# Optimization experiments

Hardware: AMD Instinct MI355X
Metric: run time of the kernel (lower is better)

## Reference

```python
import jax, jax.numpy as jnp
import numpy as np

B, L, D_IN, H, N2, NL, D_OUT = 32, 4096, 16, 128, 32, 4, 8


def setup_inputs() -> dict:
    key = jax.random.key(0)
    ks = jax.random.split(key, 12)
    x = jax.random.normal(ks[0], (B, L, D_IN), jnp.float32)
    times = jax.random.uniform(ks[1], (B, L), jnp.float32)
    enc_w = jax.random.normal(ks[2], (H, D_IN), jnp.float32) / np.sqrt(D_IN)
    enc_b = jnp.zeros((H,), jnp.float32)
    # S4D kernel params per layer (stacked along NL)
    log_dt = jax.random.uniform(ks[3], (NL, H), jnp.float32) * (np.log(0.1) - np.log(0.001)) + np.log(0.001)
    log_A_real = jnp.full((NL, H, N2), np.log(0.5), jnp.float32)
    A_imag = jnp.broadcast_to(np.pi * jnp.arange(N2, dtype=jnp.float32), (NL, H, N2)).astype(jnp.float32)
    C_re = jax.random.normal(ks[4], (NL, H, N2), jnp.float32) * (0.5 ** 0.5)
    C_im = jax.random.normal(ks[5], (NL, H, N2), jnp.float32) * (0.5 ** 0.5)
    D = jax.random.normal(ks[6], (NL, H), jnp.float32)
    conv_w = jax.random.normal(ks[7], (NL, 2 * H, H), jnp.float32) / np.sqrt(H)  # 1x1 conv
    conv_b = jnp.zeros((NL, 2 * H), jnp.float32)
    ln_w = jnp.ones((NL, H), jnp.float32)
    ln_b = jnp.zeros((NL, H), jnp.float32)
    dec_w = jax.random.normal(ks[8], (D_OUT, H), jnp.float32) / np.sqrt(H)
    dec_b = jnp.zeros((D_OUT,), jnp.float32)
    return dict(x=x, times=times, enc_w=enc_w, enc_b=enc_b, log_dt=log_dt,
                log_A_real=log_A_real, A_imag=A_imag, C_re=C_re, C_im=C_im, D=D,
                conv_w=conv_w, conv_b=conv_b, ln_w=ln_w, ln_b=ln_b, dec_w=dec_w, dec_b=dec_b)


def _s4d_kernel(log_dt, log_A_real, A_imag, C_re, C_im, L_):
    # Vandermonde construction of the S4D convolution kernel, shape (H, L)
    dt = jnp.exp(log_dt)[:, None]                      # (H, 1)
    A = -jnp.exp(log_A_real) + 1j * A_imag             # (H, N2)
    dtA = A * dt                                       # (H, N2)
    C = (C_re + 1j * C_im) * (jnp.exp(dtA) - 1.0) / A  # (H, N2)
    K = jnp.exp(dtA[:, :, None] * jnp.arange(L_))      # (H, N2, L)
    return 2.0 * jnp.einsum('hn,hnl->hl', C, K).real


def _layernorm(x, w, b, eps=1e-5):
    mu = x.mean(-1, keepdims=True)
    var = ((x - mu) ** 2).mean(-1, keepdims=True)
    return (x - mu) * jax.lax.rsqrt(var + eps) * w + b


def _forward(x, enc_w, enc_b, log_dt, log_A_real, A_imag, C_re, C_im, D,
             conv_w, conv_b, ln_w, ln_b, dec_w, dec_b):
    L_ = x.shape[1]
    u = jnp.transpose(x @ enc_w.T + enc_b, (0, 2, 1))  # (B, H, L)
    for l in range(NL):
        z = u
        k = _s4d_kernel(log_dt[l], log_A_real[l], A_imag[l], C_re[l], C_im[l], L_)  # (H, L)
        # FFT-based causal convolution with zero padding to 2L
        k_f = jnp.fft.rfft(k, n=2 * L_)                # (H, L+1)
        u_f = jnp.fft.rfft(z, n=2 * L_)                # (B, H, L+1)
        y = jnp.fft.irfft(u_f * k_f, n=2 * L_)[..., :L_]
        y = y + z * D[l][:, None]                      # skip term
        y = jax.nn.gelu(y, approximate=False)          # torch nn.GELU = exact erf
        # 1x1 conv to 2H channels then GLU over channel dim
        v = jnp.einsum('oh,bhl->bol', conv_w[l], y) + conv_b[l][:, None]
        a, g = jnp.split(v, 2, axis=1)
        y = a * jax.nn.sigmoid(g)
        u = y + u                                      # residual
        u = jnp.transpose(_layernorm(jnp.transpose(u, (0, 2, 1)), ln_w[l], ln_b[l]), (0, 2, 1))  # postnorm
    emb = jnp.transpose(u, (0, 2, 1))                  # (B, L, H)
    pooled = emb.mean(axis=1)                          # (B, H)
    pred = jax.nn.sigmoid(pooled @ dec_w.T + dec_b)    # (B, D_OUT)
    return pred, emb


def reference(x, times, enc_w, enc_b, log_dt, log_A_real, A_imag, C_re, C_im, D,
              conv_w, conv_b, ln_w, ln_b, dec_w, dec_b):
    # times is accepted but unused, matching the original forward signature
    return _forward(x, enc_w, enc_b, log_dt, log_A_real, A_imag, C_re, C_im, D,
                    conv_w, conv_b, ln_w, ln_b, dec_w, dec_b)
```

## Files before the change

kernel.cpp:

```cpp
#include <hip/hip_runtime.h>
#include <hip/hip_bf16.h>

#define B_ 32
#define L_ 4096
#define DIN 16
#define H_ 128
#define N2_ 32
#define NL_ 4
#define CL 64
#define NC 64

#define OFF_U   ((size_t)0)
#define SZ_U    ((size_t)B_*H_*L_/2)
#define OFF_Y   (OFF_U + SZ_U)
#define SZ_Y    ((size_t)B_*H_*L_/2)
#define OFF_T1  (OFF_Y + SZ_Y)
#define SZ_T1   ((size_t)NL_*H_*64*64)
#define OFF_K   (OFF_T1 + SZ_T1)
#define SZ_K    ((size_t)NL_*H_*64)
#define OFF_CP  (OFF_K + SZ_K)
#define SZ_CP   ((size_t)NL_*H_*64)
#define OFF_W64 (OFF_CP + SZ_CP)
#define SZ_W64  ((size_t)NL_*H_*64)
#define OFF_W5  (OFF_W64 + SZ_W64)
#define SZ_W5   ((size_t)NL_*H_*64)
#define OFF_DTA (OFF_W5 + SZ_W5)
#define SZ_DTA  ((size_t)NL_*H_*N2_*4)
#define OFF_PL  (OFF_DTA + SZ_DTA)
#define SZ_PL   ((size_t)B_*H_)
#define OFF_WB  (OFF_PL + SZ_PL)
#define SZ_WB   ((size_t)NL_*256*128/2)
#define OFF_T1F (OFF_WB + SZ_WB)
#define SZ_TF   ((size_t)NL_*H_*4096)
#define OFF_TKF (OFF_T1F + SZ_TF)
#define OFF_T2F (OFF_TKF + SZ_TF)

#define ZP 72
#define EP 68

typedef __bf16 bf16_t;
typedef bf16_t bf16x8 __attribute__((ext_vector_type(8)));
typedef float f32x4 __attribute__((ext_vector_type(4)));
typedef unsigned short u16x8 __attribute__((ext_vector_type(8)));

#define MFMA(a, b, c) __builtin_amdgcn_mfma_f32_16x16x32_bf16(a, b, c, 0, 0, 0)
#define BCB(v) __builtin_bit_cast(bf16x8, v)

__device__ __forceinline__ unsigned short f2bf(float f) {
    return __builtin_bit_cast(unsigned short, (__bf16)f);
}
__device__ __forceinline__ float bf2f(unsigned short u) {
    return __builtin_bit_cast(float, (unsigned int)u << 16);
}
__device__ __forceinline__ void store_hl(unsigned short* p, int idx, float v) {
    unsigned short hi = f2bf(v);
    p[idx]     = hi;
    p[idx + 8] = f2bf(v - bf2f(hi));
}
__device__ __forceinline__ float gelu_f(float a) {
    float uu = a * fmaf(0.0356774081f, a * a, 0.7978845608f);
    float e  = __expf(2.0f * uu);
    float th = 1.0f - 2.0f / (e + 1.0f);
    return 0.5f * a * (1.0f + th);
}
__device__ __forceinline__ int yswz(int l, int h) {
    return (l * 128 + h) ^ ((l & 7) << 3);
}

__global__ __launch_bounds__(256) void prep_params(const float* log_dt, const float* log_A_real,
                                                   const float* A_imag, const float* C_re,
                                                   const float* C_im, float* ws) {
    int idx = blockIdx.x * 256 + threadIdx.x;
    if (idx >= NL_ * H_ * N2_) return;
    int n  = idx & 31;
    int lh = idx >> 5;

    float dt  = expf(log_dt[lh]);
    float Are = -expf(log_A_real[idx]);
    float Aim = A_imag[idx];
    float dre = Are * dt, dim = Aim * dt;
    float er  = expf(dre);
    float sw, cw; sincosf(dim, &sw, &cw);
    float wre = er * cw, wim = er * sw;
    float nre = wre - 1.0f, nim = wim;
    float den = Are * Are + Aim * Aim;
    float qre = (nre * Are + nim * Aim) / den;
    float qim = (nim * Are - nre * Aim) / den;
    float cre = C_re[idx], cim = C_im[idx];

    float* cp  = ws + OFF_CP  + (size_t)lh * 64;
    float* w64 = ws + OFF_W64 + (size_t)lh * 64;
    float* w5  = ws + OFF_W5  + (size_t)lh * 64;
    cp[2 * n]     = cre * qre - cim * qim;
    cp[2 * n + 1] = cre * qim + cim * qre;
    *((float4*)(ws + OFF_DTA) + (size_t)lh * 32 + n) = make_float4(dre, dim, wre, wim);

    float e64 = expf(64.0f * dre);
    float s64, c64; sincosf(64.0f * dim, &s64, &c64);
    float ar = e64 * c64, ai = e64 * s64;
    w64[2 * n] = ar; w64[2 * n + 1] = ai;
    #pragma unroll
    for (int q = 0; q < 3; ++q) {
        float nr = ar * ar - ai * ai;
        float ni = 2.0f * ar * ai;
        ar = nr; ai = ni;
    }
    w5[2 * n] = ar; w5[2 * n + 1] = ai;
}

__global__ __launch_bounds__(256) void prep_pow(float* ws) {
    int idx = blockIdx.x * 256 + threadIdx.x;
    int n  = idx & 31;
    int e  = (idx >> 5) & 63;
    int lh = idx >> 11;
    float4 dw = *((const float4*)(ws + OFF_DTA) + (size_t)lh * 32 + n);
    float ew = expf((float)e * dw.x);
    float sn, cs; sincosf((float)e * dw.y, &sn, &cs);
    float pr = ew * cs, pi = ew * sn;

    float* t1 = ws + OFF_T1 + (size_t)lh * 4096;
    *(float2*)&t1[e * 64 + 2 * n] = make_float2(pr, pi);

    unsigned short* t1f = (unsigned short*)(ws + OFF_T1F) + (size_t)lh * 8192;
    unsigned short* t2f = (unsigned short*)(ws + OFF_T2F) + (size_t)lh * 8192;
    int k1 = 63 - e;
    store_hl(t1f, (k1 >> 3) * 1024 + (2 * n) * 16 + (k1 & 7), pr);
    store_hl(t1f, (k1 >> 3) * 1024 + (2 * n + 1) * 16 + (k1 & 7), pi);
    float qr = pr * dw.z - pi * dw.w;
    float qi = pr * dw.w + pi * dw.z;
    store_hl(t2f, ((2 * n) >> 3) * 1024 + e * 16 + ((2 * n) & 7), qr);
    store_hl(t2f, ((2 * n + 1) >> 3) * 1024 + e * 16 + ((2 * n + 1) & 7), qi);
}

__global__ __launch_bounds__(256) void compute_k(float* ws) {
    int idx = blockIdx.x * 256 + threadIdx.x;
    if (idx >= NL_ * H_ * 64) return;
    int s  = idx & 63;
    int lh = idx >> 6;
    const float* t1 = ws + OFF_T1 + (size_t)lh * 4096 + (size_t)s * 64;
    const float* cp = ws + OFF_CP + (size_t)lh * 64;
    float acc = 0.0f;
    #pragma unroll
    for (int n = 0; n < 32; ++n)
        acc += cp[2 * n] * t1[2 * n] - cp[2 * n + 1] * t1[2 * n + 1];
    ws[OFF_K + (size_t)lh * 64 + s] = 2.0f * acc;
}

__global__ __launch_bounds__(256) void prep_tkf(float* ws) {
    int idx = blockIdx.x * 256 + threadIdx.x;
    int tau = idx & 63;
    int s   = (idx >> 6) & 63;
    int lh  = idx >> 12;
    float v = (tau >= s) ? ws[OFF_K + (size_t)lh * 64 + (tau - s)] : 0.0f;
    unsigned short* dst = (unsigned short*)(ws + OFF_TKF) + (size_t)lh * 8192;
    store_hl(dst, (s >> 3) * 1024 + (s & 7) + tau * 16, v);
}

__global__ __launch_bounds__(256) void prep_wbf(const float* conv_w, float* ws) {
    int i = blockIdx.x * 256 + threadIdx.x;
    ((unsigned short*)(ws + OFF_WB))[i] = f2bf(conv_w[i]);
}

__global__ __launch_bounds__(256) void encoder_kernel(const float* x, const float* enc_w,
                                                      const float* enc_b, float* ws) {
    __shared__ float wlds[H_ * DIN];
    __shared__ float blds[H_];
    int t  = threadIdx.x;
    int b  = blockIdx.x >> 4;
    int l0 = (blockIdx.x & 15) * 256;
    for (int i = t; i < H_ * DIN; i += 256) wlds[i] = enc_w[i];
    if (t < H_) blds[t] = enc_b[t];
    float xr[16];
    const float* xp = x + ((size_t)b * L_ + l0 + t) * DIN;
    #pragma unroll
    for (int d = 0; d < 16; ++d) xr[d] = xp[d];
    __syncthreads();
    unsigned short* u = (unsigned short*)(ws + OFF_U) + (size_t)b * H_ * L_ + l0 + t;
    for (int h = 0; h < H_; ++h) {
        float acc = blds[h];
        #pragma unroll
        for (int d = 0; d < 16; ++d) acc += xr[d] * wlds[h * 16 + d];
        u[(size_t)h * L_] = f2bf(acc);
    }
}

__global__ __launch_bounds__(256) void s4d_mfma(const float* Dp, float* ws, int layer) {
    __shared__ unsigned short zsh[64 * ZP];
    __shared__ float eg[64 * EP];
    __shared__ float tex[8][64];
    __shared__ float bex[8][64];

    int t  = threadIdx.x;
    int b  = blockIdx.x >> 7;
    int h  = blockIdx.x & 127;
    int lh = layer * H_ + h;
    int w  = t >> 6;
    int l  = t & 63;
    int lr = l & 15;
    int lg = l >> 4;

    const unsigned short* ug = (const unsigned short*)(ws + OFF_U) + ((size_t)b * H_ + h) * L_;

    {
        int base = t * 16;
        int c = base >> 6, s0 = base & 63;
        *(u16x8*)&zsh[c * ZP + s0]     = *(const u16x8*)&ug[base];
        *(u16x8*)&zsh[c * ZP + s0 + 8] = *(const u16x8*)&ug[base + 8];
    }

    const unsigned short* t1f = (const unsigned short*)(ws + OFF_T1F) + (size_t)lh * 8192;
    const unsigned short* tkf = (const unsigned short*)(ws + OFF_TKF) + (size_t)lh * 8192;
    const unsigned short* t2f = (const unsigned short*)(ws + OFF_T2F) + (size_t)lh * 8192;
    int bo = lg * 1024 + (w * 16 + lr) * 16;
    bf16x8 T1h0 = BCB(*(const u16x8*)&t1f[bo]);
    bf16x8 T1l0 = BCB(*(const u16x8*)&t1f[bo + 8]);
    bf16x8 T1h1 = BCB(*(const u16x8*)&t1f[bo + 4096]);
    bf16x8 T1l1 = BCB(*(const u16x8*)&t1f[bo + 4096 + 8]);
    bf16x8 TKh0 = BCB(*(const u16x8*)&tkf[bo]);
    bf16x8 TKl0 = BCB(*(const u16x8*)&tkf[bo + 8]);
    bf16x8 TKh1 = BCB(*(const u16x8*)&tkf[bo + 4096]);
    bf16x8 TKl1 = BCB(*(const u16x8*)&tkf[bo + 4096 + 8]);

    f32x4 accE[4], accC[4];
    #pragma unroll
    for (int ct = 0; ct < 4; ++ct) { accE[ct] = (f32x4)0.0f; accC[ct] = (f32x4)0.0f; }

    __syncthreads();

    #pragma unroll
    for (int ct = 0; ct < 4; ++ct) {
        int ar = (ct * 16 + lr) * ZP;
        bf16x8 ah0 = BCB(*(const u16x8*)&zsh[ar + lg * 8]);
        bf16x8 ah1 = BCB(*(const u16x8*)&zsh[ar + 32 + lg * 8]);
        accE[ct] = MFMA(ah0, T1h0, accE[ct]);
        accE[ct] = MFMA(ah0, T1l0, accE[ct]);
        accE[ct] = MFMA(ah1, T1h1, accE[ct]);
        accE[ct] = MFMA(ah1, T1l1, accE[ct]);
        accC[ct] = MFMA(ah0, TKh0, accC[ct]);
        accC[ct] = MFMA(ah0, TKl0, accC[ct]);
        accC[ct] = MFMA(ah1, TKh1, accC[ct]);
        accC[ct] = MFMA(ah1, TKl1, accC[ct]);
    }
    #pragma unroll
    for (int ct = 0; ct < 4; ++ct)
        #pragma unroll
        for (int r = 0; r < 4; ++r)
            eg[(ct * 16 + lg * 4 + r) * EP + w * 16 + lr] = accE[ct][r];

    bf16x8 T2h0 = BCB(*(const u16x8*)&t2f[bo]);
    bf16x8 T2l0 = BCB(*(const u16x8*)&t2f[bo + 8]);
    bf16x8 T2h1 = BCB(*(const u16x8*)&t2f[bo + 4096]);
    bf16x8 T2l1 = BCB(*(const u16x8*)&t2f[bo + 4096 + 8]);
    float zep[16];
    #pragma unroll
    for (int ct = 0; ct < 4; ++ct)
        #pragma unroll
        for (int r = 0; r < 4; ++r) {
            int c = ct * 16 + lg * 4 + r, tau = w * 16 + lr;
            zep[ct * 4 + r] = bf2f(zsh[c * ZP + tau]);
        }
    __syncthreads();

    {
        int n   = t & 31;
        int oct = t >> 5;
        const float* cp   = ws + OFF_CP  + (size_t)lh * 64;
        const float* w64p = ws + OFF_W64 + (size_t)lh * 64;
        const float* w5p  = ws + OFF_W5  + (size_t)lh * 64;
        float cre = cp[2 * n], cim = cp[2 * n + 1];
        float wr  = w64p[2 * n], wi = w64p[2 * n + 1];
        float2 e[8];
        float sre = 0.f, sim = 0.f;
        #pragma unroll
        for (int j = 0; j < 8; ++j) {
            e[j] = *(const float2*)&eg[(8 * oct + j) * EP + 2 * n];
            float nr = fmaf(wr, sre, fmaf(-wi, sim, e[j].x));
            float ni = fmaf(wr, sim, fmaf(wi, sre, e[j].y));
            sre = nr; sim = ni;
        }
        *(float2*)&tex[oct][2 * n] = make_float2(sre, sim);
        __syncthreads();
        if (t < 32) {
            float Wr = w5p[2 * n], Wi = w5p[2 * n + 1];
            float br = 0.f, bi = 0.f;
            #pragma unroll
            for (int o = 0; o < 8; ++o) {
                *(float2*)&bex[o][2 * n] = make_float2(br, bi);
                float2 T = *(const float2*)&tex[o][2 * n];
                float nr = fmaf(Wr, br, fmaf(-Wi, bi, T.x));
                float ni = fmaf(Wr, bi, fmaf(Wi, br, T.y));
                br = nr; bi = ni;
            }
        }
        __syncthreads();
        float2 Sb = *(const float2*)&bex[oct][2 * n];
        sre = Sb.x; sim = Sb.y;
        #pragma unroll
        for (int j = 0; j < 8; ++j) {
            int c = 8 * oct + j;
            float gre = 2.0f * (cre * sre - cim * sim);
            float gim = -2.0f * (cre * sim + cim * sre);
            unsigned int pk = (unsigned int)f2bf(gre) | ((unsigned int)f2bf(gim) << 16);
            *(unsigned int*)&zsh[c * ZP + 2 * n] = pk;
            float nr = fmaf(wr, sre, fmaf(-wi, sim, e[j].x));
            float ni = fmaf(wr, sim, fmaf(wi, sre, e[j].y));
            sre = nr; sim = ni;
        }
    }
    float Dh = Dp[lh];
    __syncthreads();

    #pragma unroll
    for (int ct = 0; ct < 4; ++ct) {
        int ar = (ct * 16 + lr) * ZP;
        bf16x8 gh0 = BCB(*(const u16x8*)&zsh[ar + lg * 8]);
        bf16x8 gh1 = BCB(*(const u16x8*)&zsh[ar + 32 + lg * 8]);
        accC[ct] = MFMA(gh0, T2h0, accC[ct]);
        accC[ct] = MFMA(gh0, T2l0, accC[ct]);
        accC[ct] = MFMA(gh1, T2h1, accC[ct]);
        accC[ct] = MFMA(gh1, T2l1, accC[ct]);
    }

    unsigned short* yb = (unsigned short*)(ws + OFF_Y) + ((size_t)b * H_ + h) * L_;
    #pragma unroll
    for (int ct = 0; ct < 4; ++ct)
        #pragma unroll
        for (int r = 0; r < 4; ++r) {
            float acc = fmaf(Dh, zep[ct * 4 + r], accC[ct][r]);
            yb[(ct * 16 + lg * 4 + r) * 64 + w * 16 + lr] = f2bf(gelu_f(acc));
        }
}

__global__ __launch_bounds__(256) void conv_glu_ln_mfma(const float* conv_b, const float* ln_w,
                                                        const float* ln_b, float* ws, int layer) {
    __shared__ unsigned short yt[64 * 128];
    __shared__ float wsum[4][64];
    __shared__ float wsq[4][64];

    int t    = threadIdx.x;
    int b    = blockIdx.x >> 6;
    int l0   = (blockIdx.x & 63) * 64;
    int w    = t >> 6;
    int lam  = t & 63;
    int g4   = lam >> 4;
    int ncol = lam & 15;

    const unsigned short* yg = (const unsigned short*)(ws + OFF_Y) + (size_t)b * H_ * L_;
    const unsigned short* wb = (const unsigned short*)(ws + OFF_WB) + (size_t)layer * 256 * 128;

    {
        int ll = t & 63;
        int hb = (t >> 6) * 32;
        const unsigned short* ycol = yg + l0 + ll;
        #pragma unroll
        for (int g = 0; g < 4; ++g) {
            u16x8 tmp;
            #pragma unroll
            for (int i = 0; i < 8; ++i)
                tmp[i] = ycol[(size_t)(hb + g * 8 + i) * L_];
            *(u16x8*)&yt[yswz(ll, hb + g * 8)] = tmp;
        }
    }

    const float* cb = conv_b + layer * 256;
    f32x4 dA[2][4], dG[2][4];
    #pragma unroll
    for (int oa = 0; oa < 2; ++oa) {
        int ba = w * 32 + oa * 16 + g4 * 4;
        f32x4 bA, bG;
        #pragma unroll
        for (int r = 0; r < 4; ++r) { bA[r] = cb[ba + r]; bG[r] = cb[128 + ba + r]; }
        #pragma unroll
        for (int nt = 0; nt < 4; ++nt) { dA[oa][nt] = bA; dG[oa][nt] = bG; }
    }
    __syncthreads();

    #pragma unroll
    for (int kt = 0; kt < 4; ++kt) {
        bf16x8 aAk[2], aGk[2];
        #pragma unroll
        for (int oa = 0; oa < 2; ++oa) {
            int oA = w * 32 + oa * 16 + ncol;
            aAk[oa] = BCB(*(const u16x8*)&wb[(size_t)oA * 128 + kt * 32 + g4 * 8]);
            aGk[oa] = BCB(*(const u16x8*)&wb[(size_t)(128 + oA) * 128 + kt * 32 + g4 * 8]);
        }
        #pragma unroll
        for (int nt = 0; nt < 4; ++nt) {
            bf16x8 bfr = BCB(*(const u16x8*)&yt[yswz(nt * 16 + ncol, kt * 32 + g4 * 8)]);
            #pragma unroll
            for (int oa = 0; oa < 2; ++oa) {
                dA[oa][nt] = MFMA(aAk[oa], bfr, dA[oa][nt]);
                dG[oa][nt] = MFMA(aGk[oa], bfr, dG[oa][nt]);
            }
        }
    }

    unsigned short* ug = (unsigned short*)(ws + OFF_U) + (size_t)b * H_ * L_;
    float lwv[2][4], lbv[2][4];
    #pragma unroll
    for (int oa = 0; oa < 2; ++oa)
        #pragma unroll
        for (int r = 0; r < 4; ++r) {
            int hh = layer * 128 + w * 32 + oa * 16 + g4 * 4 + r;
            lwv[oa][r] = ln_w[hh]; lbv[oa][r] = ln_b[hh];
        }

    #pragma unroll
    for (int nt = 0; nt < 4; ++nt) {
        int l = l0 + nt * 16 + ncol;
        float s = 0.f, q = 0.f;
        #pragma unroll
        for (int oa = 0; oa < 2; ++oa)
            #pragma unroll
            for (int r = 0; r < 4; ++r) {
                int h = w * 32 + oa * 16 + g4 * 4 + r;
                float a = dA[oa][nt][r], g = dG[oa][nt][r];
                float val = a / (1.0f + __expf(-g)) + bf2f(ug[(size_t)h * L_ + l]);
                dA[oa][nt][r] = val;
                s += val; q += val * val;
            }
        s += __shfl_xor(s, 16, 64); q += __shfl_xor(q, 16, 64);
        s += __shfl_xor(s, 32, 64); q += __shfl_xor(q, 32, 64);
        if (g4 == 0) { wsum[w][nt * 16 + ncol] = s; wsq[w][nt * 16 + ncol] = q; }
    }
    __syncthreads();

    #pragma unroll
    for (int nt = 0; nt < 4; ++nt) {
        int ll = nt * 16 + ncol;
        int l  = l0 + ll;
        float S = wsum[0][ll] + wsum[1][ll] + wsum[2][ll] + wsum[3][ll];
        float Q = wsq[0][ll] + wsq[1][ll] + wsq[2][ll] + wsq[3][ll];
        float mu = S * (1.0f / 128.0f);
        float var = Q * (1.0f / 128.0f) - mu * mu;
        float rstd = rsqrtf(var + 1e-5f);
        #pragma unroll
        for (int oa = 0; oa < 2; ++oa)
            #pragma unroll
            for (int r = 0; r < 4; ++r) {
                int h = w * 32 + oa * 16 + g4 * 4 + r;
                float v = (dA[oa][nt][r] - mu) * rstd * lwv[oa][r] + lbv[oa][r];
                ug[(size_t)h * L_ + l] = f2bf(v);
            }
    }
}

__global__ __launch_bounds__(256) void pool_kernel(float* ws) {
    int bh = blockIdx.x;
    const unsigned short* u = (const unsigned short*)(ws + OFF_U) + (size_t)bh * L_;
    int t = threadIdx.x;
    float s = 0.0f;
    for (int i = t; i < L_; i += 256) s += bf2f(u[i]);
    #pragma unroll
    for (int m = 1; m <= 32; m <<= 1) s += __shfl_xor(s, m, 64);
    __shared__ float part[4];
    if ((t & 63) == 0) part[t >> 6] = s;
    __syncthreads();
    if (t == 0) ws[OFF_PL + bh] = (part[0] + part[1] + part[2] + part[3]) * (1.0f / L_);
}

__global__ __launch_bounds__(256) void decode_kernel(const float* dec_w, const float* dec_b,
                                                     const float* ws, float* out) {
    int t = threadIdx.x;
    int b = t >> 3, o = t & 7;
    const float* p = ws + OFF_PL + b * 128;
    float acc = dec_b[o];
    for (int h = 0; h < 128; ++h) acc += p[h] * dec_w[o * 128 + h];
    out[t] = 1.0f / (1.0f + __expf(-acc));
}

__global__ __launch_bounds__(256) void emb_out(const float* ws, float* out) {
    __shared__ float T[32 * 65];
    int t  = threadIdx.x;
    int bi = blockIdx.x;
    int lt = bi & 63;
    int ht = (bi >> 6) & 3;
    int b  = bi >> 8;
    int l0 = lt * 64, h0 = ht * 32;
    const unsigned short* u = (const unsigned short*)(ws + OFF_U) + ((size_t)b * H_ + h0) * L_ + l0;
    #pragma unroll
    for (int p = 0; p < 8; ++p) {
        int rr = p * 4 + (t >> 6), cc = t & 63;
        T[rr * 65 + cc] = bf2f(u[(size_t)rr * L_ + cc]);
    }
    __syncthreads();
    #pragma unroll
    for (int q = 0; q < 8; ++q) {
        int hh = t & 31, ll = (t >> 5) + q * 8;
        out[((size_t)(b * L_) + l0 + ll) * H_ + h0 + hh] = T[hh * 65 + ll];
    }
}

extern "C" void kernel_launch(void* const* d_in, const int* in_sizes, int n_in,
                              void* d_out, int out_size, void* d_ws, size_t ws_size,
                              hipStream_t stream) {
    const float* x          = (const float*)d_in[0];
    const float* enc_w      = (const float*)d_in[2];
    const float* enc_b      = (const float*)d_in[3];
    const float* log_dt     = (const float*)d_in[4];
    const float* log_A_real = (const float*)d_in[5];
    const float* A_imag     = (const float*)d_in[6];
    const float* C_re       = (const float*)d_in[7];
    const float* C_im       = (const float*)d_in[8];
    const float* Dp         = (const float*)d_in[9];
    const float* conv_w     = (const float*)d_in[10];
    const float* conv_b     = (const float*)d_in[11];
    const float* ln_w       = (const float*)d_in[12];
    const float* ln_b       = (const float*)d_in[13];
    const float* dec_w      = (const float*)d_in[14];
    const float* dec_b      = (const float*)d_in[15];
    float* ws = (float*)d_ws;
    float* out = (float*)d_out;

    prep_params<<<(NL_ * H_ * N2_ + 255) / 256, 256, 0, stream>>>(log_dt, log_A_real, A_imag,
                                                                  C_re, C_im, ws);
    prep_pow<<<(NL_ * H_ * N2_ * 64) / 256, 256, 0, stream>>>(ws);
    compute_k<<<(NL_ * H_ * 64 + 255) / 256, 256, 0, stream>>>(ws);
    prep_tkf<<<(NL_ * H_ * 64 * 64) / 256, 256, 0, stream>>>(ws);
    prep_wbf<<<(NL_ * 256 * 128) / 256, 256, 0, stream>>>(conv_w, ws);
    encoder_kernel<<<B_ * (L_ / 256), 256, 0, stream>>>(x, enc_w, enc_b, ws);
    for (int l = 0; l < NL_; ++l) {
        s4d_mfma<<<B_ * H_, 256, 0, stream>>>(Dp, ws, l);
        conv_glu_ln_mfma<<<B_ * (L_ / 64), 256, 0, stream>>>(conv_b, ln_w, ln_b, ws, l);
    }
    pool_kernel<<<B_ * H_, 256, 0, stream>>>(ws);
    decode_kernel<<<1, 256, 0, stream>>>(dec_w, dec_b, ws, out);
    emb_out<<<B_ * 4 * 64, 256, 0, stream>>>(ws, out + 256);
}
```

Baseline: 359.0 us.

## Fuse fp32 embedding output into last conv/LN layer and drop T1 table

On the last layer, the conv+GLU+layernorm kernel now writes the fp32 (B,L,H) embedding directly from the normalized values in registers. This removes the separate emb_out transpose kernel, which reread the bf16 U buffer and rewrote 64MB. compute_k now computes the Vandermonde powers on the fly with exp/sincos instead of reading a stored fp32 T1 table, so prep_pow no longer writes T1. The emitted embedding is also now the pre-bf16-rounded value, and the direct stores are float4 with a stride of H across l.

```diff
diff --git a/kernel.cpp b/kernel.cpp
--- a/kernel.cpp
+++ b/kernel.cpp
@@ -14,9 +14,7 @@
 #define SZ_U    ((size_t)B_*H_*L_/2)
 #define OFF_Y   (OFF_U + SZ_U)
 #define SZ_Y    ((size_t)B_*H_*L_/2)
-#define OFF_T1  (OFF_Y + SZ_Y)
-#define SZ_T1   ((size_t)NL_*H_*64*64)
-#define OFF_K   (OFF_T1 + SZ_T1)
+#define OFF_K   (OFF_Y + SZ_Y)
 #define SZ_K    ((size_t)NL_*H_*64)
 #define OFF_CP  (OFF_K + SZ_K)
 #define SZ_CP   ((size_t)NL_*H_*64)
@@ -118,9 +116,6 @@
     float sn, cs; sincosf((float)e * dw.y, &sn, &cs);
     float pr = ew * cs, pi = ew * sn;
 
-    float* t1 = ws + OFF_T1 + (size_t)lh * 4096;
-    *(float2*)&t1[e * 64 + 2 * n] = make_float2(pr, pi);
-
     unsigned short* t1f = (unsigned short*)(ws + OFF_T1F) + (size_t)lh * 8192;
     unsigned short* t2f = (unsigned short*)(ws + OFF_T2F) + (size_t)lh * 8192;
     int k1 = 63 - e;
@@ -137,12 +132,16 @@
     if (idx >= NL_ * H_ * 64) return;
     int s  = idx & 63;
     int lh = idx >> 6;
-    const float* t1 = ws + OFF_T1 + (size_t)lh * 4096 + (size_t)s * 64;
     const float* cp = ws + OFF_CP + (size_t)lh * 64;
+    const float4* dta = (const float4*)(ws + OFF_DTA) + (size_t)lh * 32;
     float acc = 0.0f;
-    #pragma unroll
-    for (int n = 0; n < 32; ++n)
-        acc += cp[2 * n] * t1[2 * n] - cp[2 * n + 1] * t1[2 * n + 1];
+    #pragma unroll 8
+    for (int n = 0; n < 32; ++n) {
+        float4 dw = dta[n];
+        float ew = expf((float)s * dw.x);
+        float sn, cs; sincosf((float)s * dw.y, &sn, &cs);
+        acc += cp[2 * n] * (ew * cs) - cp[2 * n + 1] * (ew * sn);
+    }
     ws[OFF_K + (size_t)lh * 64 + s] = 2.0f * acc;
 }
 
@@ -332,7 +331,8 @@
 }
 
 __global__ __launch_bounds__(256) void conv_glu_ln_mfma(const float* conv_b, const float* ln_w,
-                                                        const float* ln_b, float* ws, int layer) {
+                                                        const float* ln_b, float* ws, float* outp,
+                                                        int layer, int last) {
     __shared__ unsigned short yt[64 * 128];
     __shared__ float wsum[4][64];
     __shared__ float wsq[4][64];
@@ -435,13 +435,20 @@
         float var = Q * (1.0f / 128.0f) - mu * mu;
         float rstd = rsqrtf(var + 1e-5f);
         #pragma unroll
-        for (int oa = 0; oa < 2; ++oa)
+        for (int oa = 0; oa < 2; ++oa) {
+            float vv[4];
             #pragma unroll
             for (int r = 0; r < 4; ++r) {
                 int h = w * 32 + oa * 16 + g4 * 4 + r;
                 float v = (dA[oa][nt][r] - mu) * rstd * lwv[oa][r] + lbv[oa][r];
+                vv[r] = v;
                 ug[(size_t)h * L_ + l] = f2bf(v);
             }
+            if (last) {
+                *(float4*)&outp[((size_t)(b * L_ + l)) * H_ + w * 32 + oa * 16 + g4 * 4] =
+                    make_float4(vv[0], vv[1], vv[2], vv[3]);
+            }
+        }
     }
 }
 
@@ -467,28 +474,6 @@
     float acc = dec_b[o];
     for (int h = 0; h < 128; ++h) acc += p[h] * dec_w[o * 128 + h];
     out[t] = 1.0f / (1.0f + __expf(-acc));
-}
-
-__global__ __launch_bounds__(256) void emb_out(const float* ws, float* out) {
-    __shared__ float T[32 * 65];
-    int t  = threadIdx.x;
-    int bi = blockIdx.x;
-    int lt = bi & 63;
-    int ht = (bi >> 6) & 3;
-    int b  = bi >> 8;
-    int l0 = lt * 64, h0 = ht * 32;
-    const unsigned short* u = (const unsigned short*)(ws + OFF_U) + ((size_t)b * H_ + h0) * L_ + l0;
-    #pragma unroll
-    for (int p = 0; p < 8; ++p) {
-        int rr = p * 4 + (t >> 6), cc = t & 63;
-        T[rr * 65 + cc] = bf2f(u[(size_t)rr * L_ + cc]);
-    }
-    __syncthreads();
-    #pragma unroll
-    for (int q = 0; q < 8; ++q) {
-        int hh = t & 31, ll = (t >> 5) + q * 8;
-        out[((size_t)(b * L_) + l0 + ll) * H_ + h0 + hh] = T[hh * 65 + ll];
-    }
 }
 
 extern "C" void kernel_launch(void* const* d_in, const int* in_sizes, int n_in,
@@ -521,9 +506,9 @@
     encoder_kernel<<<B_ * (L_ / 256), 256, 0, stream>>>(x, enc_w, enc_b, ws);
     for (int l = 0; l < NL_; ++l) {
         s4d_mfma<<<B_ * H_, 256, 0, stream>>>(Dp, ws, l);
-        conv_glu_ln_mfma<<<B_ * (L_ / 64), 256, 0, stream>>>(conv_b, ln_w, ln_b, ws, l);
+        conv_glu_ln_mfma<<<B_ * (L_ / 64), 256, 0, stream>>>(conv_b, ln_w, ln_b, ws,
+                                                             out + 256, l, l == NL_ - 1);
     }
     pool_kernel<<<B_ * H_, 256, 0, stream>>>(ws);
     decode_kernel<<<1, 256, 0, stream>>>(dec_w, dec_b, ws, out);
-    emb_out<<<B_ * 4 * 64, 256, 0, stream>>>(ws, out + 256);
-}
+}
```

Measured after the change: 355.3 us, median of 2. Within noise of the previous version (-1.0%).
